# Optimization experiments

Hardware: AMD Instinct MI355X
Metric: run time of the kernel (lower is better)

Reference implementation:

```python
import jax, jax.numpy as jnp
import numpy as np

N_NODES = 50000

def _gcn_layer(x, src, dst, W, b, n_nodes):
    # x: [N, F_in]; src/dst: [E+N] (self-loops already appended)
    h = x @ W  # [N, F_out]
    deg = jax.ops.segment_sum(jnp.ones_like(dst, dtype=h.dtype), dst, num_segments=n_nodes)
    dinv = jnp.where(deg > 0, jax.lax.rsqrt(deg), 0.0)  # deg^{-1/2}
    norm = dinv[src] * dinv[dst]  # [E+N]
    msg = h[src] * norm[:, None]  # gather + scale
    out = jax.ops.segment_sum(msg, dst, num_segments=n_nodes)  # scatter-add
    return out + b

def setup_inputs() -> dict:
    key = jax.random.key(0)
    k1, k2, k3, k4 = jax.random.split(key, 4)
    d = 128
    E = 800000
    x = jax.random.normal(k1, (N_NODES, d), dtype=jnp.float32)
    edge_index = jax.random.randint(k2, (2, E), 0, N_NODES, dtype=jnp.int64)
    W1 = jax.random.normal(k3, (d, d), dtype=jnp.float32) / np.sqrt(d)
    b1 = jnp.zeros((d,), dtype=jnp.float32)
    W2 = jax.random.normal(k4, (d, d), dtype=jnp.float32) / np.sqrt(d)
    b2 = jnp.zeros((d,), dtype=jnp.float32)
    return {"x": x, "edge_index": edge_index, "W1": W1, "b1": b1, "W2": W2, "b2": b2}

def reference(x, edge_index, W1, b1, W2, b2):
    n = x.shape[0]
    loops = jnp.arange(n, dtype=edge_index.dtype)
    src = jnp.concatenate([edge_index[0], loops])  # add self-loops
    dst = jnp.concatenate([edge_index[1], loops])
    h = _gcn_layer(x, src, dst, W1, b1, n)
    h = jax.nn.relu(h)
    z = _gcn_layer(h, src, dst, W2, b2, n)
    return z
```

## Files before the change

kernel.cpp:

```cpp
#include <hip/hip_runtime.h>
#include <hip/hip_fp16.h>

#define NF 128

typedef _Float16 half8 __attribute__((ext_vector_type(8)));
typedef float    floatx4 __attribute__((ext_vector_type(4)));

__global__ __launch_bounds__(256) void prep_k(
    int* __restrict__ cnt, int n, int nb,
    const float* __restrict__ W1, const float* __restrict__ W2,
    __half* __restrict__ WT1, __half* __restrict__ WT2)
{
    int b = blockIdx.x;
    if (b < nb) {
        int i = b * 256 + threadIdx.x;
        if (i < n) cnt[i] = 0;
    } else {
        int idx = (b - nb) * 256 + threadIdx.x;
        const float* W = (idx < 16384) ? W1 : W2;
        __half* WT     = (idx < 16384) ? WT1 : WT2;
        int j = idx & 16383;
        int nn = j & 127, k = j >> 7;
        WT[nn * NF + k] = __float2half(W[k * NF + nn]);
    }
}

__global__ __launch_bounds__(256) void count_k(const int* __restrict__ dst,
                                               int* __restrict__ cnt, int E) {
    int e = (blockIdx.x * 256 + threadIdx.x) * 4;
    if (e + 3 < E) {
        int4 d = *(const int4*)(dst + e);
        atomicAdd(&cnt[d.x], 1); atomicAdd(&cnt[d.y], 1);
        atomicAdd(&cnt[d.z], 1); atomicAdd(&cnt[d.w], 1);
    } else {
        for (int k = e; k < E; k++) atomicAdd(&cnt[dst[k]], 1);
    }
}

__global__ __launch_bounds__(256) void pscan_local(
    const int* __restrict__ cnt, float* __restrict__ dinv,
    int* __restrict__ rowptr, int* __restrict__ blocksum, int n)
{
    __shared__ int sm[256];
    int tid = threadIdx.x;
    int i = blockIdx.x * 256 + tid;
    int v = (i < n) ? cnt[i] : 0;
    if (i < n) dinv[i] = rsqrtf((float)v + 1.0f);
    sm[tid] = v;
    __syncthreads();
    #pragma unroll
    for (int d = 1; d < 256; d <<= 1) {
        int t = (tid >= d) ? sm[tid - d] : 0;
        __syncthreads();
        sm[tid] += t;
        __syncthreads();
    }
    if (i < n) rowptr[i] = sm[tid] - v;
    if (tid == 255) blocksum[blockIdx.x] = sm[255];
}

__global__ __launch_bounds__(256) void add_off2(
    int* __restrict__ rowptr, int* __restrict__ cur,
    const int* __restrict__ blocksum, int n, int E, int nb)
{
    __shared__ int sm[256];
    int tid = threadIdx.x;
    sm[tid] = (tid < nb && tid < (int)blockIdx.x) ? blocksum[tid] : 0;
    __syncthreads();
    #pragma unroll
    for (int d = 128; d > 0; d >>= 1) {
        if (tid < d) sm[tid] += sm[tid + d];
        __syncthreads();
    }
    int offv = sm[0];
    int i = blockIdx.x * 256 + tid;
    if (i < n) {
        int r = rowptr[i] + offv;
        rowptr[i] = r;
        cur[i] = r;
    }
    if (blockIdx.x == 0 && tid == 0) rowptr[n] = E;
}


template<bool F32IN>
__device__ __forceinline__ void gemm_body(
    const void* __restrict__ Xv, const __half* __restrict__ WT,
    const float* __restrict__ dinv, __half* __restrict__ out, int M, int bid)
{
    __shared__ __half wlds[128][136];
    const int tid = threadIdx.x;

    {
        int r = tid >> 1;
        int c0 = (tid & 1) * 64;
        const half8* s = (const half8*)(WT + (size_t)r * NF + c0);
        half8* d = (half8*)&wlds[r][c0];
        #pragma unroll
        for (int j = 0; j < 8; j++) d[j] = s[j];
    }
    __syncthreads();

    const int wave = tid >> 6, lane = tid & 63;
    const int quad = lane >> 4, l15 = lane & 15;
    const int rowA = bid * 64 + wave * 16 + l15;
    const int rowc = (rowA < M) ? rowA : (M - 1);

    half8 afr[4];
    if (F32IN) {
        const float* X = (const float*)Xv;
        #pragma unroll
        for (int kc = 0; kc < 4; kc++) {
            const floatx4* p = (const floatx4*)(X + (size_t)rowc * NF + kc * 32 + quad * 8);
            floatx4 u = p[0], v = p[1];
            half8 a;
            a[0] = (_Float16)u[0]; a[1] = (_Float16)u[1];
            a[2] = (_Float16)u[2]; a[3] = (_Float16)u[3];
            a[4] = (_Float16)v[0]; a[5] = (_Float16)v[1];
            a[6] = (_Float16)v[2]; a[7] = (_Float16)v[3];
            afr[kc] = a;
        }
    } else {
        const __half* X = (const __half*)Xv;
        #pragma unroll
        for (int kc = 0; kc < 4; kc++)
            afr[kc] = *(const half8*)(X + (size_t)rowc * NF + kc * 32 + quad * 8);
    }

    floatx4 acc[8];
    #pragma unroll
    for (int ct = 0; ct < 8; ct++) { floatx4 z = {0.f, 0.f, 0.f, 0.f}; acc[ct] = z; }

    #pragma unroll
    for (int kc = 0; kc < 4; kc++) {
        #pragma unroll
        for (int ct = 0; ct < 8; ct++) {
            half8 b = *(const half8*)&wlds[ct * 16 + l15][kc * 32 + quad * 8];
            acc[ct] = __builtin_amdgcn_mfma_f32_16x16x32_f16(afr[kc], b, acc[ct], 0, 0, 0);
        }
    }

    const int orow0 = bid * 64 + wave * 16 + quad * 4;
    #pragma unroll
    for (int r = 0; r < 4; r++) {
        int orow = orow0 + r;
        if (orow < M) {
            float s = dinv[orow];
            #pragma unroll
            for (int ct = 0; ct < 8; ct++)
                out[(size_t)orow * NF + ct * 16 + l15] = __float2half(acc[ct][r] * s);
        }
    }
}

__global__ __launch_bounds__(256) void fill_gemm1_k(
    const int* __restrict__ src, const int* __restrict__ dst,
    int* __restrict__ cur, int* __restrict__ csr, int E, int N,
    const float* __restrict__ X, const __half* __restrict__ WT,
    const float* __restrict__ dinv, __half* __restrict__ H, int gemmBlocks)
{
    int bid = blockIdx.x;
    if (bid < gemmBlocks) {
        gemm_body<true>(X, WT, dinv, H, N, bid);
    } else {
        int b = bid - gemmBlocks;
        int part = b & 7, chunk = b >> 3;
        int e = chunk * 256 + threadIdx.x;
        int lo = (int)(((long long)part * N) >> 3);
        int hi = (int)(((long long)(part + 1) * N) >> 3);
        if (e < E) {
            int d = dst[e];
            if (d >= lo && d < hi) {
                int p = atomicAdd(&cur[d], 1);
                csr[p] = src[e];
            }
        }
    }
}

__global__ __launch_bounds__(256) void gemm2_k(
    const __half* __restrict__ A, const __half* __restrict__ WT,
    const float* __restrict__ dinv, __half* __restrict__ H, int M)
{
    gemm_body<false>(A, WT, dinv, H, M, blockIdx.x);
}


__global__ __launch_bounds__(256) void agg_k(
    const __half2* __restrict__ hs, const int* __restrict__ rowptr,
    const int* __restrict__ csr, const float* __restrict__ dinv,
    const float* __restrict__ bias, __half2* __restrict__ outh,
    float* __restrict__ outf, int n)
{
    int wave = threadIdx.x >> 6;
    int lane = threadIdx.x & 63;
    int node = blockIdx.x * 4 + wave;
    if (node >= n) return;

    const int HS = NF / 2;
    float2 acc = __half22float2(hs[(size_t)node * HS + lane]);

    int base = rowptr[node];
    int cnt  = rowptr[node + 1] - base;

    for (int off = 0; off < cnt; off += 64) {
        int m = min(64, cnt - off);
        int idx = 0;
        if (lane < m) idx = __builtin_nontemporal_load(&csr[base + off + lane]);
        int j = 0;
        for (; j + 15 < m; j += 16) {
            int s[16];
            __half2 v[16];
            #pragma unroll
            for (int t = 0; t < 16; t++) s[t] = __shfl(idx, j + t, 64);
            #pragma unroll
            for (int t = 0; t < 16; t++) v[t] = hs[(size_t)s[t] * HS + lane];
            #pragma unroll
            for (int t = 0; t < 16; t++) {
                float2 f = __half22float2(v[t]);
                acc.x += f.x; acc.y += f.y;
            }
        }
        for (; j + 3 < m; j += 4) {
            int s0 = __shfl(idx, j, 64);
            int s1 = __shfl(idx, j + 1, 64);
            int s2 = __shfl(idx, j + 2, 64);
            int s3 = __shfl(idx, j + 3, 64);
            __half2 v0 = hs[(size_t)s0 * HS + lane];
            __half2 v1 = hs[(size_t)s1 * HS + lane];
            __half2 v2 = hs[(size_t)s2 * HS + lane];
            __half2 v3 = hs[(size_t)s3 * HS + lane];
            float2 f0 = __half22float2(v0), f1 = __half22float2(v1);
            float2 f2 = __half22float2(v2), f3 = __half22float2(v3);
            acc.x += (f0.x + f1.x) + (f2.x + f3.x);
            acc.y += (f0.y + f1.y) + (f2.y + f3.y);
        }
        for (; j < m; j++) {
            int s0 = __shfl(idx, j, 64);
            float2 f0 = __half22float2(hs[(size_t)s0 * HS + lane]);
            acc.x += f0.x; acc.y += f0.y;
        }
    }

    float s = dinv[node];
    float ox = s * acc.x + bias[2 * lane];
    float oy = s * acc.y + bias[2 * lane + 1];
    if (outh) {
        ox = fmaxf(ox, 0.f); oy = fmaxf(oy, 0.f);
        outh[(size_t)node * HS + lane] = __floats2half2_rn(ox, oy);
    } else {
        ((float2*)(outf + (size_t)node * NF))[lane] = make_float2(ox, oy);
    }
}


extern "C" void kernel_launch(void* const* d_in, const int* in_sizes, int n_in,
                              void* d_out, int out_size, void* d_ws, size_t ws_size,
                              hipStream_t stream) {
    const float* x  = (const float*)d_in[0];
    const int*   ei = (const int*)d_in[1];
    const float* W1 = (const float*)d_in[2];
    const float* b1 = (const float*)d_in[3];
    const float* W2 = (const float*)d_in[4];
    const float* b2 = (const float*)d_in[5];
    float* out = (float*)d_out;

    const int N = in_sizes[0] / NF;
    const int E = in_sizes[1] / 2;
    const int* src = ei;
    const int* dst = ei + E;

    char* ws = (char*)d_ws;
    size_t off = 0;
    auto alloc = [&](size_t bytes) {
        void* p = ws + off;
        off += bytes;
        off = (off + 63) & ~(size_t)63;
        return p;
    };
    int*    cnt    = (int*)alloc((size_t)N * 4);
    int*    rowptr = (int*)alloc((size_t)(N + 1) * 4);
    int*    csr    = (int*)alloc((size_t)E * 4);
    float*  dinv   = (float*)alloc((size_t)N * 4);
    int*    bsum   = (int*)alloc((size_t)256 * 4);
    __half* WT1    = (__half*)alloc((size_t)NF * NF * 2);
    __half* WT2    = (__half*)alloc((size_t)NF * NF * 2);
    __half* H16    = (__half*)alloc((size_t)N * NF * 2);
    __half* A16    = (__half*)alloc((size_t)N * NF * 2);

    int nb = (N + 255) / 256;
    int eb = (E + 255) / 256;
    int cb = (E / 4 + 255) / 256;
    int gb = (N + 63) / 64;
    int ab = (N + 3) / 4;

    prep_k<<<nb + 128, 256, 0, stream>>>(cnt, N, nb, W1, W2, WT1, WT2);
    count_k<<<cb, 256, 0, stream>>>(dst, cnt, E);
    pscan_local<<<nb, 256, 0, stream>>>(cnt, dinv, rowptr, bsum, N);
    add_off2<<<nb, 256, 0, stream>>>(rowptr, cnt, bsum, N, E, nb);
    fill_gemm1_k<<<gb + eb * 8, 256, 0, stream>>>(src, dst, cnt, csr, E, N,
                                                  x, WT1, dinv, H16, gb);
    agg_k<<<ab, 256, 0, stream>>>((const __half2*)H16, rowptr, csr, dinv, b1,
                                  (__half2*)A16, nullptr, N);
    gemm2_k<<<gb, 256, 0, stream>>>(A16, WT2, dinv, H16, N);
    agg_k<<<ab, 256, 0, stream>>>((const __half2*)H16, rowptr, csr, dinv, b2,
                                  nullptr, out, N);
}
```

Baseline: 244.8 us.

## Split fused fill/GEMM1 kernel into separate vectorized CSR fill and GEMM kernels

Replaces the combined fill+GEMM1 kernel with two launches. In the new fill, each thread handles four edges with int4 loads and nontemporal stores. The old fill split the edge list into 8 destination-range partitions, so every edge was read eight times, presumably to improve atomic locality. Dropping that cuts the 8x redundant reads and the extra blocks, but gives up overlapping the GEMM with the fill and may scatter atomics more randomly. It also assumes E is divisible by 4 for aligned int4 loads; a scalar tail loop covers the rest.

```diff
diff --git a/kernel.cpp b/kernel.cpp
--- a/kernel.cpp
+++ b/kernel.cpp
@@ -80,6 +80,30 @@
         cur[i] = r;
     }
     if (blockIdx.x == 0 && tid == 0) rowptr[n] = E;
+}
+
+__global__ __launch_bounds__(256) void fill_k(
+    const int* __restrict__ src, const int* __restrict__ dst,
+    int* __restrict__ cur, int* __restrict__ csr, int E)
+{
+    int e = (blockIdx.x * 256 + threadIdx.x) * 4;
+    if (e + 3 < E) {
+        int4 d = *(const int4*)(dst + e);
+        int4 s = *(const int4*)(src + e);
+        int p0 = atomicAdd(&cur[d.x], 1);
+        int p1 = atomicAdd(&cur[d.y], 1);
+        int p2 = atomicAdd(&cur[d.z], 1);
+        int p3 = atomicAdd(&cur[d.w], 1);
+        __builtin_nontemporal_store(s.x, &csr[p0]);
+        __builtin_nontemporal_store(s.y, &csr[p1]);
+        __builtin_nontemporal_store(s.z, &csr[p2]);
+        __builtin_nontemporal_store(s.w, &csr[p3]);
+    } else {
+        for (int k = e; k < E; k++) {
+            int p = atomicAdd(&cur[dst[k]], 1);
+            __builtin_nontemporal_store(src[k], &csr[p]);
+        }
+    }
 }
 
 
@@ -153,29 +177,11 @@
     }
 }
 
-__global__ __launch_bounds__(256) void fill_gemm1_k(
-    const int* __restrict__ src, const int* __restrict__ dst,
-    int* __restrict__ cur, int* __restrict__ csr, int E, int N,
+__global__ __launch_bounds__(256) void gemm1_k(
     const float* __restrict__ X, const __half* __restrict__ WT,
-    const float* __restrict__ dinv, __half* __restrict__ H, int gemmBlocks)
-{
-    int bid = blockIdx.x;
-    if (bid < gemmBlocks) {
-        gemm_body<true>(X, WT, dinv, H, N, bid);
-    } else {
-        int b = bid - gemmBlocks;
-        int part = b & 7, chunk = b >> 3;
-        int e = chunk * 256 + threadIdx.x;
-        int lo = (int)(((long long)part * N) >> 3);
-        int hi = (int)(((long long)(part + 1) * N) >> 3);
-        if (e < E) {
-            int d = dst[e];
-            if (d >= lo && d < hi) {
-                int p = atomicAdd(&cur[d], 1);
-                csr[p] = src[e];
-            }
-        }
-    }
+    const float* __restrict__ dinv, __half* __restrict__ H, int M)
+{
+    gemm_body<true>(X, WT, dinv, H, M, blockIdx.x);
 }
 
 __global__ __launch_bounds__(256) void gemm2_k(
@@ -289,7 +295,6 @@
     __half* A16    = (__half*)alloc((size_t)N * NF * 2);
 
     int nb = (N + 255) / 256;
-    int eb = (E + 255) / 256;
     int cb = (E / 4 + 255) / 256;
     int gb = (N + 63) / 64;
     int ab = (N + 3) / 4;
@@ -298,8 +303,8 @@
     count_k<<<cb, 256, 0, stream>>>(dst, cnt, E);
     pscan_local<<<nb, 256, 0, stream>>>(cnt, dinv, rowptr, bsum, N);
     add_off2<<<nb, 256, 0, stream>>>(rowptr, cnt, bsum, N, E, nb);
-    fill_gemm1_k<<<gb + eb * 8, 256, 0, stream>>>(src, dst, cnt, csr, E, N,
-                                                  x, WT1, dinv, H16, gb);
+    fill_k<<<cb, 256, 0, stream>>>(src, dst, cnt, csr, E);
+    gemm1_k<<<gb, 256, 0, stream>>>(x, WT1, dinv, H16, N);
     agg_k<<<ab, 256, 0, stream>>>((const __half2*)H16, rowptr, csr, dinv, b1,
                                   (__half2*)A16, nullptr, N);
     gemm2_k<<<gb, 256, 0, stream>>>(A16, WT2, dinv, H16, N);
```

Result: slower. 266.8 us (+9.0%).
